# Performance work log

Hardware: AMD Instinct MI355X
Metric: run time of the kernel (lower is better)

Reference implementation:

```python
import jax, jax.numpy as jnp
import numpy as np

B, T, D = 4, 2048, 1024
H, HD = 16, 64  # num_heads, head_size; H*HD == D
DFF = 4 * D
EPS = 1e-5

def _ln(x, g, b):
    mu = jnp.mean(x, axis=-1, keepdims=True)
    var = jnp.mean(jnp.square(x - mu), axis=-1, keepdims=True)
    return (x - mu) * jax.lax.rsqrt(var + EPS) * g + b

def setup_inputs() -> dict:
    key = jax.random.key(0)
    ks = jax.random.split(key, 12)
    s = lambda fan_in: 1.0 / np.sqrt(fan_in)
    return {
        "x": jax.random.normal(ks[0], (B, T, D), jnp.float32),
        "Wq": jax.random.normal(ks[1], (H, D, HD), jnp.float32) * s(D),
        "Wk": jax.random.normal(ks[2], (H, D, HD), jnp.float32) * s(D),
        "Wv": jax.random.normal(ks[3], (H, D, HD), jnp.float32) * s(D),
        "Wo": jax.random.normal(ks[4], (D, D), jnp.float32) * s(D),
        "bo": jax.random.normal(ks[5], (D,), jnp.float32) * 0.01,
        "W1": jax.random.normal(ks[6], (D, DFF), jnp.float32) * s(D),
        "b1": jax.random.normal(ks[7], (DFF,), jnp.float32) * 0.01,
        "W2": jax.random.normal(ks[8], (DFF, D), jnp.float32) * s(DFF),
        "b2": jax.random.normal(ks[9], (D,), jnp.float32) * 0.01,
        "g1": jnp.ones((D,), jnp.float32),
        "be1": jnp.zeros((D,), jnp.float32),
        "g2": jnp.ones((D,), jnp.float32),
        "be2": jnp.zeros((D,), jnp.float32),
    }

def reference(x, Wq, Wk, Wv, Wo, bo, W1, b1, W2, b2, g1, be1, g2, be2):
    # pre-LN attention
    h = _ln(x, g1, be1)                                   # [B,T,D]
    q = jnp.einsum('btd,hde->bhte', h, Wq)                # [B,H,T,HD]
    k = jnp.einsum('btd,hde->bhte', h, Wk)
    v = jnp.einsum('btd,hde->bhte', h, Wv)
    scores = jnp.einsum('bhte,bhse->bhts', q, k) * (HD ** -0.5)  # [B,H,T,T]
    mask = jnp.tril(jnp.ones((T, T), bool))
    scores = jnp.where(mask, scores, -jnp.inf)
    attn = jax.nn.softmax(scores, axis=-1)
    ctx = jnp.einsum('bhts,bhse->bhte', attn, v)          # [B,H,T,HD]
    ctx = ctx.transpose(0, 2, 1, 3).reshape(B, T, D)      # concat heads
    x = x + jnp.einsum('btd,de->bte', ctx, Wo) + bo
    # pre-LN FFN
    h2 = _ln(x, g2, be2)
    ff = jax.nn.relu(jnp.einsum('btd,df->btf', h2, W1) + b1)
    x = x + jnp.einsum('btf,fd->btd', ff, W2) + b2
    return x
```

## Files before the change

kernel.cpp:

```cpp
#include <hip/hip_runtime.h>
#include <stdint.h>

#define B_ 4
#define T_ 2048
#define D_ 1024
#define H_ 16
#define HD_ 64
#define DFF_ 4096
#define M_ (B_ * T_)

typedef __bf16 bf16x8 __attribute__((ext_vector_type(8)));
typedef float f32x4 __attribute__((ext_vector_type(4)));

__device__ __forceinline__ uint16_t f2bf(float f) {
  union { float f; uint32_t u; } v;
  v.f = f;
  uint32_t r = v.u + 0x7FFF + ((v.u >> 16) & 1);
  return (uint16_t)(r >> 16);
}

#define GLD_LDS(gp, lp)                                                        \
  __builtin_amdgcn_global_load_lds(                                            \
      (const __attribute__((address_space(1))) void*)(gp),                     \
      (__attribute__((address_space(3))) void*)(lp), 16, 0, 0)

__global__ __launch_bounds__(256) void ln_bf16(const float* __restrict__ x,
                                               const float* __restrict__ gamma,
                                               const float* __restrict__ beta,
                                               uint16_t* __restrict__ out) {
  __shared__ float red[4];
  const int tid = threadIdx.x;
  const size_t row = blockIdx.x;
  const float4 v = ((const float4*)(x + row * D_))[tid];
  float s = v.x + v.y + v.z + v.w;
#pragma unroll
  for (int off = 32; off >= 1; off >>= 1) s += __shfl_xor(s, off, 64);
  if ((tid & 63) == 0) red[tid >> 6] = s;
  __syncthreads();
  const float mean = (red[0] + red[1] + red[2] + red[3]) * (1.0f / D_);
  const float d0 = v.x - mean, d1 = v.y - mean, d2 = v.z - mean, d3 = v.w - mean;
  float ss = d0 * d0 + d1 * d1 + d2 * d2 + d3 * d3;
#pragma unroll
  for (int off = 32; off >= 1; off >>= 1) ss += __shfl_xor(ss, off, 64);
  __syncthreads();
  if ((tid & 63) == 0) red[tid >> 6] = ss;
  __syncthreads();
  const float var = (red[0] + red[1] + red[2] + red[3]) * (1.0f / D_);
  const float rstd = rsqrtf(var + 1e-5f);
  const float4 g = ((const float4*)gamma)[tid];
  const float4 b = ((const float4*)beta)[tid];
  ushort4 o;
  o.x = f2bf(d0 * rstd * g.x + b.x);
  o.y = f2bf(d1 * rstd * g.y + b.y);
  o.z = f2bf(d2 * rstd * g.z + b.z);
  o.w = f2bf(d3 * rstd * g.w + b.w);
  ((ushort4*)(out + row * D_))[tid] = o;
}

__global__ __launch_bounds__(256) void transpose_cast(const float* __restrict__ in,
                                                      uint16_t* __restrict__ out,
                                                      int R, int C) {
  __shared__ float tile[32][33];
  const int tx = threadIdx.x & 31, ty = threadIdx.x >> 5;
  const int c0 = blockIdx.x * 32, r0 = blockIdx.y * 32;
#pragma unroll
  for (int i = 0; i < 32; i += 8)
    tile[ty + i][tx] = in[(size_t)(r0 + ty + i) * C + c0 + tx];
  __syncthreads();
#pragma unroll
  for (int i = 0; i < 32; i += 8)
    out[(size_t)(c0 + ty + i) * R + r0 + tx] = f2bf(tile[tx][ty + i]);
}

__global__ __launch_bounds__(256) void qkv_wt(const float* __restrict__ Wq,
                                              const float* __restrict__ Wk,
                                              const float* __restrict__ Wv,
                                              uint16_t* __restrict__ out) {
  __shared__ float tile[32][33];
  const int tx = threadIdx.x & 31, ty = threadIdx.x >> 5;
  const int z = blockIdx.z, which = z >> 4, hh = z & 15;
  const float* W = (which == 0) ? Wq : ((which == 1) ? Wk : Wv);
  const float* in = W + (size_t)hh * D_ * HD_;
  const int e0 = blockIdx.x * 32, d0 = blockIdx.y * 32;
#pragma unroll
  for (int i = 0; i < 32; i += 8)
    tile[ty + i][tx] = in[(size_t)(d0 + ty + i) * HD_ + e0 + tx];
  __syncthreads();
#pragma unroll
  for (int i = 0; i < 32; i += 8)
    out[((size_t)(which * 1024 + hh * 64) + e0 + ty + i) * D_ + d0 + tx] =
        f2bf(tile[tx][ty + i]);
}

__global__ __launch_bounds__(256) void gemm_bf16(const uint16_t* __restrict__ A,
                                                 const uint16_t* __restrict__ Bt,
                                                 void* __restrict__ C,
                                                 const float* __restrict__ bias,
                                                 const float* __restrict__ resid,
                                                 int M, int N, int K, int flags) {
  __shared__ __align__(16) uint16_t As[128 * 32];
  __shared__ __align__(16) uint16_t Bs[128 * 32];
  const int tid = threadIdx.x;
  const int lane = tid & 63, w = tid >> 6;
  const int quad = lane >> 4, lr = lane & 15;
  const int wr = w >> 1, wc = w & 1;
  const int bn0 = blockIdx.x * 128, bm0 = blockIdx.y * 128;

  f32x4 acc[4][4];
#pragma unroll
  for (int i = 0; i < 4; i++)
#pragma unroll
    for (int j = 0; j < 4; j++) acc[i][j] = f32x4{0.f, 0.f, 0.f, 0.f};

  const int s_sub = lane >> 2, s_slot = lane & 3;

  for (int k0 = 0; k0 < K; k0 += 32) {
#pragma unroll
    for (int i = 0; i < 2; i++) {
      const int r = w * 32 + i * 16 + s_sub;
      const int cg = s_slot ^ ((r >> 1) & 3);
      GLD_LDS(A + (size_t)(bm0 + r) * K + k0 + cg * 8, As + (w * 32 + i * 16) * 32);
      GLD_LDS(Bt + (size_t)(bn0 + r) * K + k0 + cg * 8, Bs + (w * 32 + i * 16) * 32);
    }
    __syncthreads();

    bf16x8 af[4], bfr[4];
#pragma unroll
    for (int i = 0; i < 4; i++) {
      const int m = wr * 64 + i * 16 + lr;
      const int slot = quad ^ ((m >> 1) & 3);
      af[i] = *(const bf16x8*)(As + m * 32 + slot * 8);
    }
#pragma unroll
    for (int j = 0; j < 4; j++) {
      const int n = wc * 64 + j * 16 + lr;
      const int slot = quad ^ ((n >> 1) & 3);
      bfr[j] = *(const bf16x8*)(Bs + n * 32 + slot * 8);
    }
#pragma unroll
    for (int i = 0; i < 4; i++)
#pragma unroll
      for (int j = 0; j < 4; j++)
        acc[i][j] = __builtin_amdgcn_mfma_f32_16x16x32_bf16(af[i], bfr[j], acc[i][j], 0, 0, 0);
    __syncthreads();
  }

  const int base_m = bm0 + wr * 64 + quad * 4;
  const int base_n = bn0 + wc * 64 + lr;
#pragma unroll
  for (int i = 0; i < 4; i++) {
#pragma unroll
    for (int j = 0; j < 4; j++) {
      const int col = base_n + j * 16;
      const float bv = bias ? bias[col] : 0.f;
#pragma unroll
      for (int r = 0; r < 4; r++) {
        const size_t row = base_m + i * 16 + r;
        float v = acc[i][j][r] + bv;
        if (resid) v += resid[row * N + col];
        if (flags & 1) v = fmaxf(v, 0.f);
        if (flags & 2)
          ((uint16_t*)C)[row * N + col] = f2bf(v);
        else
          ((float*)C)[row * N + col] = v;
      }
    }
  }
}

__global__ __launch_bounds__(256, 3) void attn_mfma(const uint16_t* __restrict__ qkv,
                                                    uint16_t* __restrict__ ctx) {
  __shared__ __align__(16) uint16_t Ks[64 * 72];
  __shared__ __align__(16) uint16_t Vt[64 * 72];
  __shared__ __align__(16) uint16_t Ps[128 * 72];
  const int tid = threadIdx.x;
  const int lane = tid & 63, w = tid >> 6;
  const int quad = lane >> 4, lr = lane & 15;
  const int tq = blockIdx.x, h = blockIdx.y, b = blockIdx.z;
  const int q0 = tq * 128;
  const uint16_t* base = qkv + (size_t)b * T_ * 3072 + h * 64;

  bf16x8 aq[2][2];
#pragma unroll
  for (int i = 0; i < 2; i++)
#pragma unroll
    for (int ks = 0; ks < 2; ks++)
      aq[i][ks] = *(const bf16x8*)(base + (size_t)(q0 + w * 32 + i * 16 + lr) * 3072 +
                                   ks * 32 + quad * 8);

  f32x4 oacc[2][4];
#pragma unroll
  for (int i = 0; i < 2; i++)
#pragma unroll
    for (int j = 0; j < 4; j++) oacc[i][j] = f32x4{0.f, 0.f, 0.f, 0.f};
  float l_part[2][4] = {{0.f, 0.f, 0.f, 0.f}, {0.f, 0.f, 0.f, 0.f}};

  const int row_min_w = q0 + w * 32;
  const int row_max_w = row_min_w + 31;
  const int nt = 2 * tq + 2;

  for (int st = 0; st < nt; st++) {
    __syncthreads();
#pragma unroll
    for (int u = 0; u < 2; u++) {
      const int uu = tid + u * 256;
      const int r = uu >> 3, c = uu & 7;
      const int4 kv = *(const int4*)(base + 1024 + (size_t)(st * 64 + r) * 3072 + c * 8);
      *(int4*)(Ks + r * 72 + c * 8) = kv;
    }
#pragma unroll
    for (int u = 0; u < 2; u++) {
      const int uu = tid + u * 256;
      const int hd = uu & 63, oct = uu >> 6;
      const uint16_t* gp = base + 2048 + (size_t)(st * 64 + oct * 8) * 3072 + hd;
      union { uint16_t u16[8]; int4 v; } tmp;
#pragma unroll
      for (int jj = 0; jj < 8; jj++) tmp.u16[jj] = gp[(size_t)jj * 3072];
      *(int4*)(Vt + hd * 72 + oct * 8) = tmp.v;
    }
    __syncthreads();

    if (st * 64 > row_max_w) continue;

    f32x4 sa[2][4];
#pragma unroll
    for (int i = 0; i < 2; i++)
#pragma unroll
      for (int j = 0; j < 4; j++) sa[i][j] = f32x4{0.f, 0.f, 0.f, 0.f};
#pragma unroll
    for (int ks = 0; ks < 2; ks++) {
      bf16x8 bk[4];
#pragma unroll
      for (int j = 0; j < 4; j++)
        bk[j] = *(const bf16x8*)(Ks + (j * 16 + lr) * 72 + ks * 32 + quad * 8);
#pragma unroll
      for (int i = 0; i < 2; i++)
#pragma unroll
        for (int j = 0; j < 4; j++)
          sa[i][j] = __builtin_amdgcn_mfma_f32_16x16x32_bf16(aq[i][ks], bk[j], sa[i][j], 0, 0, 0);
    }

    if (st * 64 + 63 > row_min_w) {
#pragma unroll
      for (int i = 0; i < 2; i++) {
        const int qrow = q0 + w * 32 + i * 16 + quad * 4;
#pragma unroll
        for (int j = 0; j < 4; j++) {
          const int col = st * 64 + j * 16 + lr;
#pragma unroll
          for (int r = 0; r < 4; r++)
            if (col > qrow + r) sa[i][j][r] = -1e30f;
        }
      }
    }

#pragma unroll
    for (int i = 0; i < 2; i++)
#pragma unroll
      for (int j = 0; j < 4; j++)
#pragma unroll
        for (int r = 0; r < 4; r++) {
          const float p = exp2f(fmaf(sa[i][j][r], 0.18033688f, -28.8539008f));
          l_part[i][r] += p;
          Ps[(size_t)(w * 32 + i * 16 + quad * 4 + r) * 72 + j * 16 + lr] = f2bf(p);
        }

#pragma unroll
    for (int ks = 0; ks < 2; ks++) {
      bf16x8 ap[2], bv[4];
#pragma unroll
      for (int i = 0; i < 2; i++)
        ap[i] = *(const bf16x8*)(Ps + (size_t)(w * 32 + i * 16 + lr) * 72 + ks * 32 + quad * 8);
#pragma unroll
      for (int j = 0; j < 4; j++)
        bv[j] = *(const bf16x8*)(Vt + (j * 16 + lr) * 72 + ks * 32 + quad * 8);
#pragma unroll
      for (int i = 0; i < 2; i++)
#pragma unroll
        for (int j = 0; j < 4; j++)
          oacc[i][j] = __builtin_amdgcn_mfma_f32_16x16x32_bf16(ap[i], bv[j], oacc[i][j], 0, 0, 0);
    }
  }

  uint16_t* ob = ctx + ((size_t)b * T_ + q0 + w * 32 + quad * 4) * D_ + h * 64 + lr;
#pragma unroll
  for (int i = 0; i < 2; i++)
#pragma unroll
    for (int r = 0; r < 4; r++) {
      float l = l_part[i][r];
#pragma unroll
      for (int dd = 1; dd < 16; dd <<= 1) l += __shfl_xor(l, dd, 64);
      const float inv = 1.f / l;
#pragma unroll
      for (int j = 0; j < 4; j++)
        ob[(size_t)(i * 16 + r) * D_ + j * 16] = f2bf(oacc[i][j][r] * inv);
    }
}

extern "C" void kernel_launch(void* const* d_in, const int* in_sizes, int n_in,
                              void* d_out, int out_size, void* d_ws, size_t ws_size,
                              hipStream_t stream) {
  const float* x = (const float*)d_in[0];
  const float* Wq = (const float*)d_in[1];
  const float* Wk = (const float*)d_in[2];
  const float* Wv = (const float*)d_in[3];
  const float* Wo = (const float*)d_in[4];
  const float* bo = (const float*)d_in[5];
  const float* W1 = (const float*)d_in[6];
  const float* b1 = (const float*)d_in[7];
  const float* W2 = (const float*)d_in[8];
  const float* b2 = (const float*)d_in[9];
  const float* g1 = (const float*)d_in[10];
  const float* be1 = (const float*)d_in[11];
  const float* g2 = (const float*)d_in[12];
  const float* be2 = (const float*)d_in[13];
  float* out = (float*)d_out;

  const size_t MB = 1024ull * 1024ull;
  if (ws_size < 200 * MB) return;
  char* ws = (char*)d_ws;
  uint16_t* hbuf = (uint16_t*)(ws + 0 * MB);
  uint16_t* wqkvt = (uint16_t*)(ws + 16 * MB);
  uint16_t* wot = (uint16_t*)(ws + 22 * MB);
  uint16_t* w1t = (uint16_t*)(ws + 24 * MB);
  uint16_t* w2t = (uint16_t*)(ws + 32 * MB);
  float* x1 = (float*)(ws + 40 * MB);
  uint16_t* qkvb = (uint16_t*)(ws + 72 * MB);
  uint16_t* ctxb = (uint16_t*)(ws + 120 * MB);
  uint16_t* ffb = (uint16_t*)(ws + 136 * MB);

  qkv_wt<<<dim3(2, 32, 48), 256, 0, stream>>>(Wq, Wk, Wv, wqkvt);
  transpose_cast<<<dim3(32, 32), 256, 0, stream>>>(Wo, wot, 1024, 1024);
  transpose_cast<<<dim3(128, 32), 256, 0, stream>>>(W1, w1t, 1024, 4096);
  transpose_cast<<<dim3(32, 128), 256, 0, stream>>>(W2, w2t, 4096, 1024);

  ln_bf16<<<M_, 256, 0, stream>>>(x, g1, be1, hbuf);
  gemm_bf16<<<dim3(24, 64), 256, 0, stream>>>(hbuf, wqkvt, qkvb, nullptr, nullptr,
                                              M_, 3 * D_, D_, 2);
  attn_mfma<<<dim3(T_ / 128, H_, B_), 256, 0, stream>>>(qkvb, ctxb);
  gemm_bf16<<<dim3(8, 64), 256, 0, stream>>>(ctxb, wot, x1, bo, x, M_, D_, D_, 0);
  ln_bf16<<<M_, 256, 0, stream>>>(x1, g2, be2, hbuf);
  gemm_bf16<<<dim3(32, 64), 256, 0, stream>>>(hbuf, w1t, ffb, b1, nullptr, M_, DFF_,
                                              D_, 1 | 2);
  gemm_bf16<<<dim3(8, 64), 256, 0, stream>>>(ffb, w2t, out, b2, x1, M_, D_, DFF_, 0);
}
```

Before: 651.4 us.

## Pre-transpose V, pair causal query tiles per block, swap QK operand order

```diff
diff --git a/kernel.cpp b/kernel.cpp
--- a/kernel.cpp
+++ b/kernel.cpp
@@ -168,133 +168,167 @@
   }
 }
 
-__global__ __launch_bounds__(256, 3) void attn_mfma(const uint16_t* __restrict__ qkv,
-                                                    uint16_t* __restrict__ ctx) {
+__global__ __launch_bounds__(256) void v_transpose(const uint16_t* __restrict__ qkv,
+                                                   uint16_t* __restrict__ vtb) {
+  __shared__ __align__(16) uint16_t tile[64 * 72];
+  const int tid = threadIdx.x;
+  const int t0 = blockIdx.x * 64;
+  const int bh = blockIdx.y;
+  const int b = bh >> 4, h = bh & 15;
+  const uint16_t* src = qkv + (size_t)b * T_ * 3072 + 2048 + h * 64;
+#pragma unroll
+  for (int u = 0; u < 2; u++) {
+    const int uu = tid + u * 256;
+    const int r = uu >> 3, c = uu & 7;
+    *(int4*)(tile + r * 72 + c * 8) =
+        *(const int4*)(src + (size_t)(t0 + r) * 3072 + c * 8);
+  }
+  __syncthreads();
+  uint16_t* dst = vtb + ((size_t)bh * 64) * T_ + t0;
+#pragma unroll
+  for (int u = 0; u < 2; u++) {
+    const int uu = tid + u * 256;
+    const int e = uu >> 3, c2 = uu & 7;
+    union { uint16_t u16[8]; int4 v; } tmp;
+#pragma unroll
+    for (int jj = 0; jj < 8; jj++) tmp.u16[jj] = tile[(c2 * 8 + jj) * 72 + e];
+    *(int4*)(dst + (size_t)e * T_ + c2 * 8) = tmp.v;
+  }
+}
+
+__global__ __launch_bounds__(256) void attn_mfma(const uint16_t* __restrict__ qkv,
+                                                 const uint16_t* __restrict__ vtb,
+                                                 uint16_t* __restrict__ ctx) {
   __shared__ __align__(16) uint16_t Ks[64 * 72];
   __shared__ __align__(16) uint16_t Vt[64 * 72];
   __shared__ __align__(16) uint16_t Ps[128 * 72];
   const int tid = threadIdx.x;
   const int lane = tid & 63, w = tid >> 6;
   const int quad = lane >> 4, lr = lane & 15;
-  const int tq = blockIdx.x, h = blockIdx.y, b = blockIdx.z;
-  const int q0 = tq * 128;
+  const int h = blockIdx.y, b = blockIdx.z;
   const uint16_t* base = qkv + (size_t)b * T_ * 3072 + h * 64;
-
-  bf16x8 aq[2][2];
-#pragma unroll
-  for (int i = 0; i < 2; i++)
-#pragma unroll
-    for (int ks = 0; ks < 2; ks++)
-      aq[i][ks] = *(const bf16x8*)(base + (size_t)(q0 + w * 32 + i * 16 + lr) * 3072 +
-                                   ks * 32 + quad * 8);
-
-  f32x4 oacc[2][4];
-#pragma unroll
-  for (int i = 0; i < 2; i++)
-#pragma unroll
-    for (int j = 0; j < 4; j++) oacc[i][j] = f32x4{0.f, 0.f, 0.f, 0.f};
-  float l_part[2][4] = {{0.f, 0.f, 0.f, 0.f}, {0.f, 0.f, 0.f, 0.f}};
-
-  const int row_min_w = q0 + w * 32;
-  const int row_max_w = row_min_w + 31;
-  const int nt = 2 * tq + 2;
-
-  for (int st = 0; st < nt; st++) {
-    __syncthreads();
-#pragma unroll
-    for (int u = 0; u < 2; u++) {
-      const int uu = tid + u * 256;
-      const int r = uu >> 3, c = uu & 7;
-      const int4 kv = *(const int4*)(base + 1024 + (size_t)(st * 64 + r) * 3072 + c * 8);
-      *(int4*)(Ks + r * 72 + c * 8) = kv;
-    }
-#pragma unroll
-    for (int u = 0; u < 2; u++) {
-      const int uu = tid + u * 256;
-      const int hd = uu & 63, oct = uu >> 6;
-      const uint16_t* gp = base + 2048 + (size_t)(st * 64 + oct * 8) * 3072 + hd;
-      union { uint16_t u16[8]; int4 v; } tmp;
-#pragma unroll
-      for (int jj = 0; jj < 8; jj++) tmp.u16[jj] = gp[(size_t)jj * 3072];
-      *(int4*)(Vt + hd * 72 + oct * 8) = tmp.v;
-    }
-    __syncthreads();
-
-    if (st * 64 > row_max_w) continue;
-
-    f32x4 sa[2][4];
+  const uint16_t* vbase = vtb + ((size_t)(b * H_ + h) * 64) * T_;
+  const int sr = tid >> 3, sc = tid & 7;
+
+#pragma unroll
+  for (int half = 0; half < 2; half++) {
+    const int tq = (half == 0) ? (int)blockIdx.x : 15 - (int)blockIdx.x;
+    const int q0 = tq * 128;
+
+    bf16x8 aq[2][2];
 #pragma unroll
     for (int i = 0; i < 2; i++)
 #pragma unroll
-      for (int j = 0; j < 4; j++) sa[i][j] = f32x4{0.f, 0.f, 0.f, 0.f};
-#pragma unroll
-    for (int ks = 0; ks < 2; ks++) {
-      bf16x8 bk[4];
-#pragma unroll
-      for (int j = 0; j < 4; j++)
-        bk[j] = *(const bf16x8*)(Ks + (j * 16 + lr) * 72 + ks * 32 + quad * 8);
+      for (int ks = 0; ks < 2; ks++)
+        aq[i][ks] = *(const bf16x8*)(base + (size_t)(q0 + w * 32 + i * 16 + lr) * 3072 +
+                                     ks * 32 + quad * 8);
+
+    f32x4 oacc[2][4];
+#pragma unroll
+    for (int i = 0; i < 2; i++)
+#pragma unroll
+      for (int j = 0; j < 4; j++) oacc[i][j] = f32x4{0.f, 0.f, 0.f, 0.f};
+    float l_part[2] = {0.f, 0.f};
+
+    const int row_min_w = q0 + w * 32;
+    const int row_max_w = row_min_w + 31;
+    const int nt = 2 * tq + 2;
+
+    for (int st = 0; st < nt; st++) {
+      __syncthreads();
+#pragma unroll
+      for (int u = 0; u < 2; u++) {
+        const int r = sr + u * 32;
+        *(int4*)(Ks + r * 72 + sc * 8) =
+            *(const int4*)(base + 1024 + (size_t)(st * 64 + r) * 3072 + sc * 8);
+        *(int4*)(Vt + r * 72 + sc * 8) =
+            *(const int4*)(vbase + (size_t)r * T_ + st * 64 + sc * 8);
+      }
+      __syncthreads();
+
+      if (st * 64 > row_max_w) continue;
+
+      f32x4 sa[2][4];
 #pragma unroll
       for (int i = 0; i < 2; i++)
 #pragma unroll
+        for (int sf = 0; sf < 4; sf++) sa[i][sf] = f32x4{0.f, 0.f, 0.f, 0.f};
+#pragma unroll
+      for (int ks = 0; ks < 2; ks++) {
+        bf16x8 ak[4];
+#pragma unroll
+        for (int sf = 0; sf < 4; sf++)
+          ak[sf] = *(const bf16x8*)(Ks + (sf * 16 + lr) * 72 + ks * 32 + quad * 8);
+#pragma unroll
+        for (int i = 0; i < 2; i++)
+#pragma unroll
+          for (int sf = 0; sf < 4; sf++)
+            sa[i][sf] = __builtin_amdgcn_mfma_f32_16x16x32_bf16(ak[sf], aq[i][ks],
+                                                                sa[i][sf], 0, 0, 0);
+      }
+
+#pragma unroll
+      for (int i = 0; i < 2; i++) {
+        const int mrow = q0 + w * 32 + i * 16 + lr;
+#pragma unroll
+        for (int sf = 0; sf < 4; sf++) {
+          const int s0 = st * 64 + sf * 16 + quad * 4;
+          float p[4];
+#pragma unroll
+          for (int r = 0; r < 4; r++) {
+            float sv = sa[i][sf][r];
+            if (s0 + r > mrow) sv = -1e30f;
+            p[r] = exp2f(fmaf(sv, 0.18033688f, -28.8539008f));
+            l_part[i] += p[r];
+          }
+          ushort4 pk;
+          pk.x = f2bf(p[0]);
+          pk.y = f2bf(p[1]);
+          pk.z = f2bf(p[2]);
+          pk.w = f2bf(p[3]);
+          *(ushort4*)(Ps + (size_t)(w * 32 + i * 16 + lr) * 72 + sf * 16 + quad * 4) = pk;
+        }
+      }
+
+#pragma unroll
+      for (int ks = 0; ks < 2; ks++) {
+        bf16x8 ap[2], bv[4];
+#pragma unroll
+        for (int i = 0; i < 2; i++)
+          ap[i] = *(const bf16x8*)(Ps + (size_t)(w * 32 + i * 16 + lr) * 72 + ks * 32 +
+                                   quad * 8);
+#pragma unroll
         for (int j = 0; j < 4; j++)
-          sa[i][j] = __builtin_amdgcn_mfma_f32_16x16x32_bf16(aq[i][ks], bk[j], sa[i][j], 0, 0, 0);
-    }
-
-    if (st * 64 + 63 > row_min_w) {
-#pragma unroll
-      for (int i = 0; i < 2; i++) {
-        const int qrow = q0 + w * 32 + i * 16 + quad * 4;
-#pragma unroll
-        for (int j = 0; j < 4; j++) {
-          const int col = st * 64 + j * 16 + lr;
-#pragma unroll
-          for (int r = 0; r < 4; r++)
-            if (col > qrow + r) sa[i][j][r] = -1e30f;
-        }
-      }
-    }
-
+          bv[j] = *(const bf16x8*)(Vt + (j * 16 + lr) * 72 + ks * 32 + quad * 8);
+#pragma unroll
+        for (int i = 0; i < 2; i++)
+#pragma unroll
+          for (int j = 0; j < 4; j++)
+            oacc[i][j] =
+                __builtin_amdgcn_mfma_f32_16x16x32_bf16(ap[i], bv[j], oacc[i][j], 0, 0, 0);
+      }
+    }
+
+    float linv[2];
+#pragma unroll
+    for (int i = 0; i < 2; i++) {
+      float l = l_part[i];
+      l += __shfl_xor(l, 16, 64);
+      l += __shfl_xor(l, 32, 64);
+      linv[i] = 1.f / l;
+    }
+    uint16_t* ob =
+        ctx + ((size_t)b * T_ + q0 + w * 32 + quad * 4) * D_ + h * 64 + lr;
 #pragma unroll
     for (int i = 0; i < 2; i++)
 #pragma unroll
-      for (int j = 0; j < 4; j++)
-#pragma unroll
-        for (int r = 0; r < 4; r++) {
-          const float p = exp2f(fmaf(sa[i][j][r], 0.18033688f, -28.8539008f));
-          l_part[i][r] += p;
-          Ps[(size_t)(w * 32 + i * 16 + quad * 4 + r) * 72 + j * 16 + lr] = f2bf(p);
-        }
-
-#pragma unroll
-    for (int ks = 0; ks < 2; ks++) {
-      bf16x8 ap[2], bv[4];
-#pragma unroll
-      for (int i = 0; i < 2; i++)
-        ap[i] = *(const bf16x8*)(Ps + (size_t)(w * 32 + i * 16 + lr) * 72 + ks * 32 + quad * 8);
-#pragma unroll
-      for (int j = 0; j < 4; j++)
-        bv[j] = *(const bf16x8*)(Vt + (j * 16 + lr) * 72 + ks * 32 + quad * 8);
-#pragma unroll
-      for (int i = 0; i < 2; i++)
+      for (int r = 0; r < 4; r++) {
+        const float inv = __shfl(linv[i], quad * 4 + r, 64);
 #pragma unroll
         for (int j = 0; j < 4; j++)
-          oacc[i][j] = __builtin_amdgcn_mfma_f32_16x16x32_bf16(ap[i], bv[j], oacc[i][j], 0, 0, 0);
-    }
-  }
-
-  uint16_t* ob = ctx + ((size_t)b * T_ + q0 + w * 32 + quad * 4) * D_ + h * 64 + lr;
-#pragma unroll
-  for (int i = 0; i < 2; i++)
-#pragma unroll
-    for (int r = 0; r < 4; r++) {
-      float l = l_part[i][r];
-#pragma unroll
-      for (int dd = 1; dd < 16; dd <<= 1) l += __shfl_xor(l, dd, 64);
-      const float inv = 1.f / l;
-#pragma unroll
-      for (int j = 0; j < 4; j++)
-        ob[(size_t)(i * 16 + r) * D_ + j * 16] = f2bf(oacc[i][j][r] * inv);
-    }
+          ob[(size_t)(i * 16 + r) * D_ + j * 16] = f2bf(oacc[i][j][r] * inv);
+      }
+  }
 }
 
 extern "C" void kernel_launch(void* const* d_in, const int* in_sizes, int n_in,
@@ -327,6 +361,7 @@
   float* x1 = (float*)(ws + 40 * MB);
   uint16_t* qkvb = (uint16_t*)(ws + 72 * MB);
   uint16_t* ctxb = (uint16_t*)(ws + 120 * MB);
+  uint16_t* vtb = (uint16_t*)(ws + 136 * MB);
   uint16_t* ffb = (uint16_t*)(ws + 136 * MB);
 
   qkv_wt<<<dim3(2, 32, 48), 256, 0, stream>>>(Wq, Wk, Wv, wqkvt);
@@ -337,7 +372,8 @@
   ln_bf16<<<M_, 256, 0, stream>>>(x, g1, be1, hbuf);
   gemm_bf16<<<dim3(24, 64), 256, 0, stream>>>(hbuf, wqkvt, qkvb, nullptr, nullptr,
                                               M_, 3 * D_, D_, 2);
-  attn_mfma<<<dim3(T_ / 128, H_, B_), 256, 0, stream>>>(qkvb, ctxb);
+  v_transpose<<<dim3(T_ / 64, B_ * H_), 256, 0, stream>>>(qkvb, vtb);
+  attn_mfma<<<dim3(8, H_, B_), 256, 0, stream>>>(qkvb, vtb, ctxb);
   gemm_bf16<<<dim3(8, 64), 256, 0, stream>>>(ctxb, wot, x1, bo, x, M_, D_, D_, 0);
   ln_bf16<<<M_, 256, 0, stream>>>(x1, g2, be2, hbuf);
   gemm_bf16<<<dim3(32, 64), 256, 0, stream>>>(hbuf, w1t, ffb, b1, nullptr, M_, DFF_,
```

Result: faster. 629.2 us (-3.4%).
